# Kernel optimization log

Measured on AMD Instinct MI355X. Metric: run time of the kernel, lower is better.

Reference implementation:

```python
import jax, jax.numpy as jnp
import numpy as np

N_NODES = 50000


def gcn_conv(x, src, dst, W, b, n_nodes):
    """PyG GCNConv: self-loops + symmetric normalization D^-1/2 (A+I) D^-1/2 X W + b."""
    loop = jnp.arange(n_nodes, dtype=src.dtype)
    s = jnp.concatenate([src, loop])
    d = jnp.concatenate([dst, loop])
    deg = jax.ops.segment_sum(jnp.ones_like(d, dtype=x.dtype), d, num_segments=n_nodes)
    dinv = jnp.where(deg > 0, jax.lax.rsqrt(deg), 0.0)
    norm = dinv[s] * dinv[d]  # (E+N,)
    h = x @ W  # (N, out)
    msg = h[s] * norm[:, None]
    return jax.ops.segment_sum(msg, d, num_segments=n_nodes) + b


def setup_inputs() -> dict:
    key = jax.random.key(0)
    ks = jax.random.split(key, 16)
    N, S, D = N_NODES, 20, 128
    E = 1_600_000
    PH, PO, GH, GO = 64, 128, 128, 32

    def lin(k, fan_in, fan_out):
        bound = 1.0 / np.sqrt(fan_in)
        kw, kb = jax.random.split(k)
        W = jax.random.uniform(kw, (fan_in, fan_out), jnp.float32, -bound, bound)
        b = jax.random.uniform(kb, (fan_out,), jnp.float32, -bound, bound)
        return W, b

    W_embed, b_embed = lin(ks[0], D, PH)
    W_attn, b_attn = lin(ks[1], PH, 1)
    W_out, b_out = lin(ks[2], PH, PO)
    W1, b1 = lin(ks[3], PO, GH)
    W2, b2 = lin(ks[4], GH, GO)
    Wm1, bm1 = lin(ks[5], GO, 64)
    Wm2, bm2 = lin(ks[6], 64, 1)

    return {
        "set_features": jax.random.normal(ks[7], (N, S, D), jnp.float32),
        "set_mask": jnp.ones((N, S), jnp.int32),
        "edge_index": jax.random.randint(ks[8], (2, E), 0, N, jnp.int32),
        "query_idx": jax.random.randint(ks[9], (4096,), 0, N, jnp.int32),
        "W_embed": W_embed, "b_embed": b_embed,
        "W_attn": W_attn, "b_attn": b_attn,
        "W_out": W_out, "b_out": b_out,
        "W1": W1, "b1": b1, "W2": W2, "b2": b2,
        "Wm1": Wm1, "bm1": bm1, "Wm2": Wm2, "bm2": bm2,
    }


def reference(set_features, set_mask, edge_index, query_idx,
              W_embed, b_embed, W_attn, b_attn, W_out, b_out,
              W1, b1, W2, b2, Wm1, bm1, Wm2, bm2):
    n_nodes = set_features.shape[0]
    # Attention pooling over each node's set: (N, S, D) -> (N, PO)
    z = jax.nn.relu(set_features @ W_embed + b_embed)          # (N, S, PH)
    scores = (z @ W_attn)[..., 0] + b_attn[0]                  # (N, S)
    scores = jnp.where(set_mask == 0, -jnp.inf, scores)
    attn = jax.nn.softmax(scores, axis=1)                      # (N, S)
    pooled = jnp.einsum('nsh,ns->nh', z, attn) @ W_out + b_out  # (N, PO)

    src, dst = edge_index[0], edge_index[1]
    x = jax.nn.relu(gcn_conv(pooled, src, dst, W1, b1, n_nodes))
    x = jax.nn.relu(gcn_conv(x, src, dst, W2, b2, n_nodes))

    q = x[query_idx]                                            # (B, GO)
    logits = (jax.nn.relu(q @ Wm1 + bm1) @ Wm2 + bm2)[..., 0]   # (B,)
    return logits
```

## Files before the change

### kernel.cpp

```cpp
#include <hip/hip_runtime.h>
#include <math.h>

#define RFL(x) __builtin_amdgcn_readfirstlane(x)
#define RL(x, l) __int_as_float(__builtin_amdgcn_readlane(__float_as_int(x), (l)))

typedef __attribute__((ext_vector_type(8))) short bf16x8;
typedef __attribute__((ext_vector_type(4))) float f32x4;

__device__ inline unsigned short bf16_rne(float f) {
  unsigned u = __float_as_uint(f);
  u += 0x7FFFu + ((u >> 16) & 1u);
  return (unsigned short)(u >> 16);
}


__global__ __launch_bounds__(256) void k_zero(int* p, int n) {
  int t = blockIdx.x * 256 + threadIdx.x;
  if (t < n) p[t] = 0;
}

__global__ __launch_bounds__(256) void k_count(const int* __restrict__ dst, int* cnt, int E) {
  int stride = gridDim.x * blockDim.x;
  for (int e = blockIdx.x * blockDim.x + threadIdx.x; e < E; e += stride)
    atomicAdd(&cnt[dst[e]], 1);
}


__global__ __launch_bounds__(256) void k_scan1(const int* __restrict__ cnt, int* __restrict__ row,
                                               int* __restrict__ partial, int N) {
  __shared__ int sm[256];
  int t = threadIdx.x, g = blockIdx.x * 256 + t;
  int v = (g < N) ? cnt[g] : 0;
  sm[t] = v;
  __syncthreads();
#pragma unroll
  for (int off = 1; off < 256; off <<= 1) {
    int x = 0;
    if (t >= off) x = sm[t - off];
    __syncthreads();
    if (t >= off) sm[t] += x;
    __syncthreads();
  }
  if (g < N) row[g] = sm[t] - v;
  if (t == 255) partial[blockIdx.x] = sm[255];
}

__global__ __launch_bounds__(256) void k_scan2(int* __restrict__ partial, int P) {
  __shared__ int sm[256];
  int t = threadIdx.x;
  int carry = 0;
  for (int base = 0; base < P; base += 256) {
    int idx = base + t;
    int v = (idx < P) ? partial[idx] : 0;
    sm[t] = v;
    __syncthreads();
#pragma unroll
    for (int off = 1; off < 256; off <<= 1) {
      int x = 0;
      if (t >= off) x = sm[t - off];
      __syncthreads();
      if (t >= off) sm[t] += x;
      __syncthreads();
    }
    if (idx < P) partial[idx] = carry + sm[t] - v;
    int tot = sm[255];
    __syncthreads();
    carry += tot;
  }
}

__global__ __launch_bounds__(256) void k_scan3(int* __restrict__ row, const int* __restrict__ partial,
                                               int* __restrict__ cursor, const int* __restrict__ cnt,
                                               float* __restrict__ dinv, int N) {
  int g = blockIdx.x * 256 + threadIdx.x;
  if (g < N) {
    int v = row[g] + partial[blockIdx.x];
    row[g] = v;
    cursor[g] = v;
    dinv[g] = rsqrtf((float)cnt[g] + 1.0f);
  }
}


__global__ __launch_bounds__(256) void k_edge_fill(const int* __restrict__ src, const int* __restrict__ dst,
                                                   int* __restrict__ cursor, int* __restrict__ esrc, int E) {
  int stride = gridDim.x * blockDim.x;
  for (int e = blockIdx.x * blockDim.x + threadIdx.x; e < E; e += stride) {
    int s = src[e], d = dst[e];
    int pos = atomicAdd(&cursor[d], 1);
    esrc[pos] = s;
  }
}


__global__ __launch_bounds__(256) void k_wc(const float* __restrict__ Wout, const float* __restrict__ bout,
                                            const float* __restrict__ W1, float* __restrict__ Wc,
                                            float* __restrict__ bc) {
  int t = blockIdx.x * 256 + threadIdx.x;
  if (t >= 65 * 128) return;
  int h = t >> 7, o = t & 127;
  const float* row = (h < 64) ? (Wout + h * 128) : bout;
  float a = 0.f;
  for (int d = 0; d < 128; ++d) a += row[d] * W1[d * 128 + o];
  if (h < 64) Wc[h * 128 + o] = a;
  else bc[o] = a;
}


__global__ __launch_bounds__(256, 3) void k_pool(const float* __restrict__ X, const int* __restrict__ mask,
                                                 const float* __restrict__ WE, const float* __restrict__ bE,
                                                 const float* __restrict__ WA, const float* __restrict__ bA,
                                                 float* __restrict__ pz, int N) {
  __shared__ __align__(16) unsigned short Xh[80][136];
  __shared__ __align__(16) unsigned short Xl[80][136];
  __shared__ float scorep[80][4];
  __shared__ float sco[80];
  __shared__ float wgtA[80];
  float* zt = (float*)&Xh[0][0];

  const int t = threadIdx.x;
  const int lane = t & 63;
  const int wv = t >> 6;
  const int cb = wv * 16;
  const int l16 = lane & 15;
  const int lg = lane >> 4;

  const long long totRows = (long long)N * 20;
  const int numTiles = (N + 3) / 4;

  const int r0 = t >> 5;
  const int kq4 = (t & 31) * 4;

  bf16x8 bh[4], bl[4];
#pragma unroll
  for (int kk = 0; kk < 4; ++kk) {
    union { bf16x8 v; unsigned short s[8]; } uh, ul;
#pragma unroll
    for (int i = 0; i < 8; ++i) {
      int k = kk * 32 + lg * 8 + i;
      float w = WE[k * 64 + cb + l16];
      unsigned short h = bf16_rne(w);
      uh.s[i] = h;
      ul.s[i] = bf16_rne(w - __uint_as_float((unsigned)h << 16));
    }
    bh[kk] = uh.v;
    bl[kk] = ul.v;
  }
  const float bEv = bE[cb + l16];
  const float WAv = WA[cb + l16];
  const float bAv = bA[0];
  const float NEG = -3.0e38f;

  int tile = blockIdx.x;
  if (tile >= numTiles) return;

  float4 xv[10];
#pragma unroll
  for (int q = 0; q < 10; ++q) {
    long long rr = (long long)tile * 80 + r0 + q * 8;
    if (rr >= totRows) rr = totRows - 1;
    xv[q] = *(const float4*)(X + rr * 128 + kq4);
  }
  int mkcur = 1;
  {
    long long mi = (long long)tile * 80 + t;
    if (t < 80) mkcur = (mi < totRows) ? mask[mi] : 0;
  }

  while (true) {
#pragma unroll
    for (int q = 0; q < 10; ++q) {
      const int r = r0 + q * 8;
      const float4 v = xv[q];
      unsigned short h0 = bf16_rne(v.x), h1 = bf16_rne(v.y), h2 = bf16_rne(v.z), h3 = bf16_rne(v.w);
      float f0 = __uint_as_float((unsigned)h0 << 16);
      float f1 = __uint_as_float((unsigned)h1 << 16);
      float f2 = __uint_as_float((unsigned)h2 << 16);
      float f3 = __uint_as_float((unsigned)h3 << 16);
      *(ushort4*)&Xh[r][kq4] = make_ushort4(h0, h1, h2, h3);
      *(ushort4*)&Xl[r][kq4] = make_ushort4(bf16_rne(v.x - f0), bf16_rne(v.y - f1),
                                            bf16_rne(v.z - f2), bf16_rne(v.w - f3));
    }
    __syncthreads();

    const int nextTile = tile + gridDim.x;
    const bool hasNext = nextTile < numTiles;
    float4 xn[10];
    int mknext = 1;
    {
      const long long nb = (long long)(hasNext ? nextTile : tile) * 80;
#pragma unroll
      for (int q = 0; q < 10; ++q) {
        long long rr = nb + r0 + q * 8;
        if (rr >= totRows) rr = totRows - 1;
        xn[q] = *(const float4*)(X + rr * 128 + kq4);
      }
      long long mi = nb + t;
      if (t < 80) mknext = (mi < totRows) ? mask[mi] : 0;
    }

    f32x4 acc[5];
#pragma unroll
    for (int rt = 0; rt < 5; ++rt) acc[rt] = (f32x4){0.f, 0.f, 0.f, 0.f};
#pragma unroll
    for (int rt = 0; rt < 5; ++rt) {
      const int rl = rt * 16 + l16;
#pragma unroll
      for (int kk = 0; kk < 4; ++kk) {
        const int ko = kk * 32 + lg * 8;
        bf16x8 ah = *(const bf16x8*)&Xh[rl][ko];
        bf16x8 al = *(const bf16x8*)&Xl[rl][ko];
        acc[rt] = __builtin_amdgcn_mfma_f32_16x16x32_bf16(ah, bh[kk], acc[rt], 0, 0, 0);
        acc[rt] = __builtin_amdgcn_mfma_f32_16x16x32_bf16(ah, bl[kk], acc[rt], 0, 0, 0);
        acc[rt] = __builtin_amdgcn_mfma_f32_16x16x32_bf16(al, bh[kk], acc[rt], 0, 0, 0);
      }
    }

#pragma unroll
    for (int rt = 0; rt < 5; ++rt) {
#pragma unroll
      for (int j = 0; j < 4; ++j) {
        float z = fmaxf(acc[rt][j] + bEv, 0.f);
        acc[rt][j] = z;
        float v = z * WAv;
        v += __shfl_xor(v, 1, 64);
        v += __shfl_xor(v, 2, 64);
        v += __shfl_xor(v, 4, 64);
        v += __shfl_xor(v, 8, 64);
        if (l16 == 0) scorep[rt * 16 + lg * 4 + j][wv] = v;
      }
    }
    __syncthreads();

#pragma unroll
    for (int rt = 0; rt < 5; ++rt) {
#pragma unroll
      for (int j = 0; j < 4; ++j) {
        int row = rt * 16 + lg * 4 + j;
        zt[row * 68 + cb + l16] = acc[rt][j];
      }
    }
    if (t < 80) {
      float4 sp = *(const float4*)scorep[t];
      float sc = sp.x + sp.y + sp.z + sp.w + bAv;
      if (mkcur == 0) sc = NEG;
      sco[t] = sc;
    }
    __syncthreads();

    if (t < 80) {
      const int base = (t / 20) * 20;
      float mx = NEG;
#pragma unroll
      for (int i = 0; i < 20; ++i) mx = fmaxf(mx, sco[base + i]);
      float den = 0.f;
#pragma unroll
      for (int i = 0; i < 20; ++i) den += __expf(sco[base + i] - mx);
      wgtA[t] = __expf(sco[t] - mx) / den;
    }
    __syncthreads();

    {
      int n = t >> 6, col = t & 63;
      float s = 0.f;
#pragma unroll
      for (int i = 0; i < 20; ++i) s += zt[(n * 20 + i) * 68 + col] * wgtA[n * 20 + i];
      long long node = (long long)tile * 4 + n;
      if (node < N) pz[node * 64 + col] = s;
    }

    if (!hasNext) break;
    __syncthreads();
#pragma unroll
    for (int q = 0; q < 10; ++q) xv[q] = xn[q];
    mkcur = mknext;
    tile = nextTile;
  }
}


__global__ __launch_bounds__(256, 2) void k_gemm1(const float* __restrict__ pz, const float* __restrict__ Wc,
                                                  const float* __restrict__ bc, const float* __restrict__ dinv,
                                                  float* __restrict__ h1p, int N) {
  const int lane = threadIdx.x & 63;
  float w0[64], w1[64];
#pragma unroll
  for (int d = 0; d < 64; ++d) {
    w0[d] = Wc[d * 128 + lane];
    w1[d] = Wc[d * 128 + 64 + lane];
  }
  const float b0 = bc[lane], b1v = bc[64 + lane];
  const int nw = (gridDim.x * blockDim.x) >> 6;
  const int w_id = (blockIdx.x * blockDim.x + threadIdx.x) >> 6;
  for (int r = w_id; r < N; r += nw) {
    const float xv = pz[(size_t)r * 64 + lane];
    const int xi = __float_as_int(xv);
    float p0 = 0.f, p1 = 0.f, p2 = 0.f, p3 = 0.f;
#pragma unroll
    for (int d0 = 0; d0 < 64; d0 += 2) {
      float a0 = RL((float&)xi, d0);
      float a1 = RL((float&)xi, d0 + 1);
      p0 += a0 * w0[d0];
      p1 += a0 * w1[d0];
      p2 += a1 * w0[d0 + 1];
      p3 += a1 * w1[d0 + 1];
    }
    float di = dinv[r];
    size_t o = (size_t)r * 128 + lane;
    h1p[o] = (b0 + p0 + p2) * di;
    h1p[o + 64] = (b1v + p1 + p3) * di;
  }
}


__global__ __launch_bounds__(256) void k_gather1(const int* __restrict__ row, const int* __restrict__ cnt,
                                                 const int* __restrict__ esrc, const float* __restrict__ h1p,
                                                 const float* __restrict__ dinv, float* __restrict__ x1, int N) {
  const int lane = threadIdx.x & 63;
  const int node = RFL(blockIdx.x * 4 + (threadIdx.x >> 6));
  if (node >= N) return;
  const int half = lane >> 5, f4 = lane & 31;
  const int rs = RFL(row[node]);
  const int ne = RFL(cnt[node]);
  const float di = dinv[node];
  const float4* __restrict__ hv = (const float4*)h1p;
  float a0 = 0.f, a1 = 0.f, a2 = 0.f, a3 = 0.f;
  int j = 0;
  for (; j + 16 <= ne; j += 16) {
    const int b = rs + j + half * 8;
    int s[8];
#pragma unroll
    for (int u = 0; u < 8; ++u) s[u] = esrc[b + u];
    float4 v[8];
#pragma unroll
    for (int u = 0; u < 8; ++u) v[u] = hv[(size_t)s[u] * 32 + f4];
#pragma unroll
    for (int u = 0; u < 8; ++u) {
      a0 += v[u].x; a1 += v[u].y; a2 += v[u].z; a3 += v[u].w;
    }
  }
  if (j < ne) {
    const int b = j + half * 8;
    int s[8];
    float m[8];
#pragma unroll
    for (int u = 0; u < 8; ++u) {
      int idx = b + u;
      int c = (idx < ne) ? idx : (ne - 1);
      s[u] = esrc[rs + c];
      m[u] = (idx < ne) ? 1.f : 0.f;
    }
    float4 v[8];
#pragma unroll
    for (int u = 0; u < 8; ++u) v[u] = hv[(size_t)s[u] * 32 + f4];
#pragma unroll
    for (int u = 0; u < 8; ++u) {
      a0 += v[u].x * m[u]; a1 += v[u].y * m[u]; a2 += v[u].z * m[u]; a3 += v[u].w * m[u];
    }
  }
  a0 += __shfl_xor(a0, 32, 64);
  a1 += __shfl_xor(a1, 32, 64);
  a2 += __shfl_xor(a2, 32, 64);
  a3 += __shfl_xor(a3, 32, 64);
  if (half == 0) {
    float4 sv = hv[(size_t)node * 32 + f4];
    float4 o;
    o.x = (a0 + sv.x * di) * di;
    o.y = (a1 + sv.y * di) * di;
    o.z = (a2 + sv.z * di) * di;
    o.w = (a3 + sv.w * di) * di;
    ((float4*)x1)[(size_t)node * 32 + f4] = o;
  }
}


__global__ __launch_bounds__(256, 2) void k_gemm2(const float* __restrict__ x1, const float* __restrict__ b1,
                                                  const float* __restrict__ W2, const float* __restrict__ dinv,
                                                  float* __restrict__ h2p, int N) {
  const int lane = threadIdx.x & 63;
  const int col = lane & 31;
  float w[128];
#pragma unroll
  for (int d = 0; d < 128; ++d) w[d] = W2[d * 32 + col];
  const float bb0 = b1[lane], bb1 = b1[64 + lane];
  const int nw = (gridDim.x * blockDim.x) >> 6;
  const int w_id = (blockIdx.x * blockDim.x + threadIdx.x) >> 6;
  for (int r = w_id; r < N; r += nw) {
    float rx0 = fmaxf(x1[(size_t)r * 128 + lane] + bb0, 0.f);
    float rx1 = fmaxf(x1[(size_t)r * 128 + 64 + lane] + bb1, 0.f);
    const int xi0 = __float_as_int(rx0), xi1 = __float_as_int(rx1);
    float p0 = 0.f, p1 = 0.f, p2 = 0.f, p3 = 0.f;
#pragma unroll
    for (int d0 = 0; d0 < 64; d0 += 2) {
      float a0 = RL((float&)xi0, d0);
      float a1 = RL((float&)xi0, d0 + 1);
      float c0 = RL((float&)xi1, d0);
      float c1 = RL((float&)xi1, d0 + 1);
      p0 += a0 * w[d0];
      p1 += a1 * w[d0 + 1];
      p2 += c0 * w[64 + d0];
      p3 += c1 * w[64 + d0 + 1];
    }
    if (lane < 32) {
      float di = dinv[r];
      h2p[(size_t)r * 32 + col] = ((p0 + p1) + (p2 + p3)) * di;
    }
  }
}


__global__ __launch_bounds__(256) void k_gather2(const int* __restrict__ row, const int* __restrict__ cnt,
                                                 const int* __restrict__ esrc, const float* __restrict__ h2p,
                                                 const float* __restrict__ dinv, float* __restrict__ x2, int N) {
  const int lane = threadIdx.x & 63;
  const int node = RFL(blockIdx.x * 4 + (threadIdx.x >> 6));
  if (node >= N) return;
  const int q = lane >> 3, f4 = lane & 7;
  const int rs = RFL(row[node]);
  const int ne = RFL(cnt[node]);
  const float di = dinv[node];
  const float4* __restrict__ hv = (const float4*)h2p;
  float a0 = 0.f, a1 = 0.f, a2 = 0.f, a3 = 0.f;
  int j = 0;
  for (; j + 32 <= ne; j += 32) {
    const int b = rs + j + q * 4;
    int s[4];
#pragma unroll
    for (int u = 0; u < 4; ++u) s[u] = esrc[b + u];
    float4 v[4];
#pragma unroll
    for (int u = 0; u < 4; ++u) v[u] = hv[(size_t)s[u] * 8 + f4];
#pragma unroll
    for (int u = 0; u < 4; ++u) {
      a0 += v[u].x; a1 += v[u].y; a2 += v[u].z; a3 += v[u].w;
    }
  }
  if (j < ne) {
    const int b = j + q * 4;
    int s[4];
    float m[4];
#pragma unroll
    for (int u = 0; u < 4; ++u) {
      int idx = b + u;
      int c = (idx < ne) ? idx : (ne - 1);
      s[u] = esrc[rs + c];
      m[u] = (idx < ne) ? 1.f : 0.f;
    }
    float4 v[4];
#pragma unroll
    for (int u = 0; u < 4; ++u) v[u] = hv[(size_t)s[u] * 8 + f4];
#pragma unroll
    for (int u = 0; u < 4; ++u) {
      a0 += v[u].x * m[u]; a1 += v[u].y * m[u]; a2 += v[u].z * m[u]; a3 += v[u].w * m[u];
    }
  }
#pragma unroll
  for (int off = 8; off <= 32; off <<= 1) {
    a0 += __shfl_xor(a0, off, 64);
    a1 += __shfl_xor(a1, off, 64);
    a2 += __shfl_xor(a2, off, 64);
    a3 += __shfl_xor(a3, off, 64);
  }
  if (q == 0) {
    float4 sv = hv[(size_t)node * 8 + f4];
    float4 o;
    o.x = (a0 + sv.x * di) * di;
    o.y = (a1 + sv.y * di) * di;
    o.z = (a2 + sv.z * di) * di;
    o.w = (a3 + sv.w * di) * di;
    ((float4*)x2)[(size_t)node * 8 + f4] = o;
  }
}


__global__ __launch_bounds__(256) void k_mlp(const int* __restrict__ qidx, const float* __restrict__ x2,
                                             const float* __restrict__ b2, const float* __restrict__ Wm1,
                                             const float* __restrict__ bm1, const float* __restrict__ Wm2,
                                             const float* __restrict__ bm2, float* __restrict__ out, int B) {
  int t = blockIdx.x * 256 + threadIdx.x;
  if (t >= B) return;
  int n = qidx[t];
  float qv[32];
#pragma unroll
  for (int k = 0; k < 32; ++k) qv[k] = fmaxf(x2[(size_t)n * 32 + k] + b2[k], 0.f);
  float acc = bm2[0];
  for (int j = 0; j < 64; ++j) {
    float h = bm1[j];
#pragma unroll
    for (int k = 0; k < 32; ++k) h += qv[k] * Wm1[k * 64 + j];
    acc += fmaxf(h, 0.f) * Wm2[j];
  }
  out[t] = acc;
}


extern "C" void kernel_launch(void* const* d_in, const int* in_sizes, int n_in,
                              void* d_out, int out_size, void* d_ws, size_t ws_size,
                              hipStream_t stream) {
  const float* X    = (const float*)d_in[0];
  const int*   mask = (const int*)d_in[1];
  const int*   ei   = (const int*)d_in[2];
  const int*   qidx = (const int*)d_in[3];
  const float* WE   = (const float*)d_in[4];
  const float* bE   = (const float*)d_in[5];
  const float* WA   = (const float*)d_in[6];
  const float* bA   = (const float*)d_in[7];
  const float* Wout = (const float*)d_in[8];
  const float* bout = (const float*)d_in[9];
  const float* W1   = (const float*)d_in[10];
  const float* b1   = (const float*)d_in[11];
  const float* W2   = (const float*)d_in[12];
  const float* b2   = (const float*)d_in[13];
  const float* Wm1  = (const float*)d_in[14];
  const float* bm1  = (const float*)d_in[15];
  const float* Wm2  = (const float*)d_in[16];
  const float* bm2  = (const float*)d_in[17];

  const int N = in_sizes[1] / 20;
  const int E = in_sizes[2] / 2;
  const int B = in_sizes[3];
  const int* src  = ei;
  const int* dstp = ei + E;

  const size_t Na = ((size_t)N + 63) & ~(size_t)63;
  const size_t Ea = ((size_t)E + 63) & ~(size_t)63;
  const int P = (N + 255) / 256;
  const size_t Pa = ((size_t)P + 63) & ~(size_t)63;

  float* ws      = (float*)d_ws;
  float* dinv    = ws;
  int*   cnt     = (int*)(dinv + Na);
  int*   rowp    = cnt + Na;
  int*   cursor  = rowp + Na;
  int*   partial = cursor + Na;
  int*   esrc    = partial + Pa;
  float* Wc      = (float*)(esrc + Ea);
  float* bc      = Wc + 8192;
  float* pz      = bc + 128;
  float* h1p     = pz + (size_t)N * 64;
  float* x1      = h1p + (size_t)N * 128;
  float* h2p     = pz;
  float* x2      = pz + (size_t)N * 32;

  const int nb = (N + 255) / 256;
  const int nw4 = (N + 3) / 4;
  const int poolBlocks = ((N + 3) / 4 < 768) ? (N + 3) / 4 : 768;

  k_zero<<<nb, 256, 0, stream>>>(cnt, N);
  k_count<<<1024, 256, 0, stream>>>(dstp, cnt, E);
  k_scan1<<<P, 256, 0, stream>>>(cnt, rowp, partial, N);
  k_scan2<<<1, 256, 0, stream>>>(partial, P);
  k_scan3<<<P, 256, 0, stream>>>(rowp, partial, cursor, cnt, dinv, N);
  k_edge_fill<<<1024, 256, 0, stream>>>(src, dstp, cursor, esrc, E);
  k_wc<<<33, 256, 0, stream>>>(Wout, bout, W1, Wc, bc);
  k_pool<<<poolBlocks, 256, 0, stream>>>(X, mask, WE, bE, WA, bA, pz, N);
  k_gemm1<<<1024, 256, 0, stream>>>(pz, Wc, bc, dinv, h1p, N);
  k_gather1<<<nw4, 256, 0, stream>>>(rowp, cnt, esrc, h1p, dinv, x1, N);
  k_gemm2<<<1024, 256, 0, stream>>>(x1, b1, W2, dinv, h2p, N);
  k_gather2<<<nw4, 256, 0, stream>>>(rowp, cnt, esrc, h2p, dinv, x2, N);
  k_mlp<<<(B + 255) / 256, 256, 0, stream>>>(qidx, x2, b2, Wm1, bm1, Wm2, bm2, (float*)d_out, B);
}
```

Before: 564.2 us.

## Aggregate 64-wide pooled features before first GCN linear transform

Reorders the first GCN layer so that neighbour aggregation runs on the 64-dimensional pooled features (pre-scaled by dinv in the pooling kernel) and the combined Wout·W1 linear map is applied afterwards. The bias term is handled by also aggregating the neighbour dinv values into a per-node scalar that multiplies the bias. This halves the bytes gathered per edge in the first gather pass, at the cost of an extra per-edge dinv load and a scalar reduction.

```diff
diff --git a/kernel.cpp b/kernel.cpp
--- a/kernel.cpp
+++ b/kernel.cpp
@@ -110,7 +110,7 @@
 __global__ __launch_bounds__(256, 3) void k_pool(const float* __restrict__ X, const int* __restrict__ mask,
                                                  const float* __restrict__ WE, const float* __restrict__ bE,
                                                  const float* __restrict__ WA, const float* __restrict__ bA,
-                                                 float* __restrict__ pz, int N) {
+                                                 const float* __restrict__ dinv, float* __restrict__ pzp, int N) {
   __shared__ __align__(16) unsigned short Xh[80][136];
   __shared__ __align__(16) unsigned short Xl[80][136];
   __shared__ float scorep[80][4];
@@ -262,11 +262,13 @@
 
     {
       int n = t >> 6, col = t & 63;
-      float s = 0.f;
-#pragma unroll
-      for (int i = 0; i < 20; ++i) s += zt[(n * 20 + i) * 68 + col] * wgtA[n * 20 + i];
       long long node = (long long)tile * 4 + n;
-      if (node < N) pz[node * 64 + col] = s;
+      if (node < N) {
+        float s = 0.f;
+#pragma unroll
+        for (int i = 0; i < 20; ++i) s += zt[(n * 20 + i) * 68 + col] * wgtA[n * 20 + i];
+        pzp[node * 64 + col] = s * dinv[node];
+      }
     }
 
     if (!hasNext) break;
@@ -279,9 +281,75 @@
 }
 
 
-__global__ __launch_bounds__(256, 2) void k_gemm1(const float* __restrict__ pz, const float* __restrict__ Wc,
-                                                  const float* __restrict__ bc, const float* __restrict__ dinv,
-                                                  float* __restrict__ h1p, int N) {
+__global__ __launch_bounds__(256) void k_gather1(const int* __restrict__ row, const int* __restrict__ cnt,
+                                                 const int* __restrict__ esrc, const float* __restrict__ pzp,
+                                                 const float* __restrict__ dinv, float* __restrict__ y,
+                                                 float* __restrict__ gout, int N) {
+  const int lane = threadIdx.x & 63;
+  const int node = RFL(blockIdx.x * 4 + (threadIdx.x >> 6));
+  if (node >= N) return;
+  const int q = lane >> 4, f4 = lane & 15;
+  const int rs = RFL(row[node]);
+  const int ne = RFL(cnt[node]);
+  const float di = dinv[node];
+  const float4* __restrict__ hv = (const float4*)pzp;
+  float a0 = 0.f, a1 = 0.f, a2 = 0.f, a3 = 0.f, ds = 0.f;
+  int j = 0;
+  for (; j + 16 <= ne; j += 16) {
+    const int b = rs + j + q * 4;
+    int s[4];
+#pragma unroll
+    for (int u = 0; u < 4; ++u) s[u] = esrc[b + u];
+    float4 v[4];
+#pragma unroll
+    for (int u = 0; u < 4; ++u) v[u] = hv[(size_t)s[u] * 16 + f4];
+#pragma unroll
+    for (int u = 0; u < 4; ++u) {
+      a0 += v[u].x; a1 += v[u].y; a2 += v[u].z; a3 += v[u].w;
+      ds += dinv[s[u]];
+    }
+  }
+  if (j < ne) {
+    const int b = j + q * 4;
+    int s[4];
+    float m[4];
+#pragma unroll
+    for (int u = 0; u < 4; ++u) {
+      int idx = b + u;
+      int c = (idx < ne) ? idx : (ne - 1);
+      s[u] = esrc[rs + c];
+      m[u] = (idx < ne) ? 1.f : 0.f;
+    }
+    float4 v[4];
+#pragma unroll
+    for (int u = 0; u < 4; ++u) v[u] = hv[(size_t)s[u] * 16 + f4];
+#pragma unroll
+    for (int u = 0; u < 4; ++u) {
+      a0 += v[u].x * m[u]; a1 += v[u].y * m[u]; a2 += v[u].z * m[u]; a3 += v[u].w * m[u];
+      ds += dinv[s[u]] * m[u];
+    }
+  }
+  a0 += __shfl_xor(a0, 16, 64); a0 += __shfl_xor(a0, 32, 64);
+  a1 += __shfl_xor(a1, 16, 64); a1 += __shfl_xor(a1, 32, 64);
+  a2 += __shfl_xor(a2, 16, 64); a2 += __shfl_xor(a2, 32, 64);
+  a3 += __shfl_xor(a3, 16, 64); a3 += __shfl_xor(a3, 32, 64);
+  ds += __shfl_xor(ds, 16, 64); ds += __shfl_xor(ds, 32, 64);
+  if (lane < 16) {
+    float4 sv = hv[(size_t)node * 16 + f4];
+    float4 o;
+    o.x = (a0 + sv.x * di) * di;
+    o.y = (a1 + sv.y * di) * di;
+    o.z = (a2 + sv.z * di) * di;
+    o.w = (a3 + sv.w * di) * di;
+    ((float4*)y)[(size_t)node * 16 + f4] = o;
+    if (f4 == 0) gout[node] = di * (ds + di * di);
+  }
+}
+
+
+__global__ __launch_bounds__(256, 2) void k_gemm1(const float* __restrict__ y, const float* __restrict__ gin,
+                                                  const float* __restrict__ Wc, const float* __restrict__ bc,
+                                                  float* __restrict__ x1, int N) {
   const int lane = threadIdx.x & 63;
   float w0[64], w1[64];
 #pragma unroll
@@ -293,7 +361,8 @@
   const int nw = (gridDim.x * blockDim.x) >> 6;
   const int w_id = (blockIdx.x * blockDim.x + threadIdx.x) >> 6;
   for (int r = w_id; r < N; r += nw) {
-    const float xv = pz[(size_t)r * 64 + lane];
+    const float xv = y[(size_t)r * 64 + lane];
+    const float gr = gin[r];
     const int xi = __float_as_int(xv);
     float p0 = 0.f, p1 = 0.f, p2 = 0.f, p3 = 0.f;
 #pragma unroll
@@ -305,71 +374,9 @@
       p2 += a1 * w0[d0 + 1];
       p3 += a1 * w1[d0 + 1];
     }
-    float di = dinv[r];
     size_t o = (size_t)r * 128 + lane;
-    h1p[o] = (b0 + p0 + p2) * di;
-    h1p[o + 64] = (b1v + p1 + p3) * di;
-  }
-}
-
-
-__global__ __launch_bounds__(256) void k_gather1(const int* __restrict__ row, const int* __restrict__ cnt,
-                                                 const int* __restrict__ esrc, const float* __restrict__ h1p,
-                                                 const float* __restrict__ dinv, float* __restrict__ x1, int N) {
-  const int lane = threadIdx.x & 63;
-  const int node = RFL(blockIdx.x * 4 + (threadIdx.x >> 6));
-  if (node >= N) return;
-  const int half = lane >> 5, f4 = lane & 31;
-  const int rs = RFL(row[node]);
-  const int ne = RFL(cnt[node]);
-  const float di = dinv[node];
-  const float4* __restrict__ hv = (const float4*)h1p;
-  float a0 = 0.f, a1 = 0.f, a2 = 0.f, a3 = 0.f;
-  int j = 0;
-  for (; j + 16 <= ne; j += 16) {
-    const int b = rs + j + half * 8;
-    int s[8];
-#pragma unroll
-    for (int u = 0; u < 8; ++u) s[u] = esrc[b + u];
-    float4 v[8];
-#pragma unroll
-    for (int u = 0; u < 8; ++u) v[u] = hv[(size_t)s[u] * 32 + f4];
-#pragma unroll
-    for (int u = 0; u < 8; ++u) {
-      a0 += v[u].x; a1 += v[u].y; a2 += v[u].z; a3 += v[u].w;
-    }
-  }
-  if (j < ne) {
-    const int b = j + half * 8;
-    int s[8];
-    float m[8];
-#pragma unroll
-    for (int u = 0; u < 8; ++u) {
-      int idx = b + u;
-      int c = (idx < ne) ? idx : (ne - 1);
-      s[u] = esrc[rs + c];
-      m[u] = (idx < ne) ? 1.f : 0.f;
-    }
-    float4 v[8];
-#pragma unroll
-    for (int u = 0; u < 8; ++u) v[u] = hv[(size_t)s[u] * 32 + f4];
-#pragma unroll
-    for (int u = 0; u < 8; ++u) {
-      a0 += v[u].x * m[u]; a1 += v[u].y * m[u]; a2 += v[u].z * m[u]; a3 += v[u].w * m[u];
-    }
-  }
-  a0 += __shfl_xor(a0, 32, 64);
-  a1 += __shfl_xor(a1, 32, 64);
-  a2 += __shfl_xor(a2, 32, 64);
-  a3 += __shfl_xor(a3, 32, 64);
-  if (half == 0) {
-    float4 sv = hv[(size_t)node * 32 + f4];
-    float4 o;
-    o.x = (a0 + sv.x * di) * di;
-    o.y = (a1 + sv.y * di) * di;
-    o.z = (a2 + sv.z * di) * di;
-    o.w = (a3 + sv.w * di) * di;
-    ((float4*)x1)[(size_t)node * 32 + f4] = o;
+    x1[o] = p0 + p2 + gr * b0;
+    x1[o + 64] = p1 + p3 + gr * b1v;
   }
 }
 
@@ -536,11 +543,12 @@
   int*   esrc    = partial + Pa;
   float* Wc      = (float*)(esrc + Ea);
   float* bc      = Wc + 8192;
-  float* pz      = bc + 128;
-  float* h1p     = pz + (size_t)N * 64;
-  float* x1      = h1p + (size_t)N * 128;
-  float* h2p     = pz;
-  float* x2      = pz + (size_t)N * 32;
+  float* gbuf    = bc + 128;
+  float* pzp     = gbuf + Na;
+  float* y       = pzp + (size_t)N * 64;
+  float* x1      = y + (size_t)N * 64;
+  float* h2p     = pzp;
+  float* x2      = pzp + (size_t)N * 32;
 
   const int nb = (N + 255) / 256;
   const int nw4 = (N + 3) / 4;
@@ -553,9 +561,9 @@
   k_scan3<<<P, 256, 0, stream>>>(rowp, partial, cursor, cnt, dinv, N);
   k_edge_fill<<<1024, 256, 0, stream>>>(src, dstp, cursor, esrc, E);
   k_wc<<<33, 256, 0, stream>>>(Wout, bout, W1, Wc, bc);
-  k_pool<<<poolBlocks, 256, 0, stream>>>(X, mask, WE, bE, WA, bA, pz, N);
-  k_gemm1<<<1024, 256, 0, stream>>>(pz, Wc, bc, dinv, h1p, N);
-  k_gather1<<<nw4, 256, 0, stream>>>(rowp, cnt, esrc, h1p, dinv, x1, N);
+  k_pool<<<poolBlocks, 256, 0, stream>>>(X, mask, WE, bE, WA, bA, dinv, pzp, N);
+  k_gather1<<<nw4, 256, 0, stream>>>(rowp, cnt, esrc, pzp, dinv, y, gbuf, N);
+  k_gemm1<<<1024, 256, 0, stream>>>(y, gbuf, Wc, bc, x1, N);
   k_gemm2<<<1024, 256, 0, stream>>>(x1, b1, W2, dinv, h2p, N);
   k_gather2<<<nw4, 256, 0, stream>>>(rowp, cnt, esrc, h2p, dinv, x2, N);
   k_mlp<<<(B + 255) / 256, 256, 0, stream>>>(qidx, x2, b2, Wm1, bm1, Wm2, bm2, (float*)d_out, B);
```

After: 510.5 us. 9.5% less time.
